# Optimization experiments

Hardware: AMD Instinct MI355X
Metric: run time of the kernel (lower is better)

The kernel has to match this reference:

```python
import jax, jax.numpy as jnp
import numpy as np

H = 16           # num_heads
D = 1024         # hidden_size
HD = D // H      # head_dim = 64
LN_EPS = 1e-5


def setup_inputs() -> dict:
    key = jax.random.key(0)
    ks = jax.random.split(key, 11)
    s = 1.0 / np.sqrt(D)
    x = jax.random.normal(ks[0], (2, 2048, D), dtype=jnp.float32)
    Wq = jax.random.uniform(ks[1], (D, D), jnp.float32, -s, s)
    bq = jax.random.uniform(ks[2], (D,), jnp.float32, -s, s)
    Wk = jax.random.uniform(ks[3], (D, D), jnp.float32, -s, s)
    bk = jax.random.uniform(ks[4], (D,), jnp.float32, -s, s)
    Wv = jax.random.uniform(ks[5], (D, D), jnp.float32, -s, s)
    bv = jax.random.uniform(ks[6], (D,), jnp.float32, -s, s)
    Wo = jax.random.uniform(ks[7], (D, D), jnp.float32, -s, s)
    bo = jax.random.uniform(ks[8], (D,), jnp.float32, -s, s)
    gamma = jnp.ones((D,), jnp.float32)
    beta = jnp.zeros((D,), jnp.float32)
    return {"x": x, "Wq": Wq, "bq": bq, "Wk": Wk, "bk": bk,
            "Wv": Wv, "bv": bv, "Wo": Wo, "bo": bo,
            "gamma": gamma, "beta": beta}


def reference(x, Wq, bq, Wk, bk, Wv, bv, Wo, bo, gamma, beta):
    B, S, _ = x.shape
    # projections -> [B, H, S, HD]
    def split_heads(t):
        return t.reshape(B, S, H, HD).transpose(0, 2, 1, 3)
    Q = split_heads(x @ Wq + bq)
    K = split_heads(x @ Wk + bk)
    V = split_heads(x @ Wv + bv)
    # scores [B, H, S, S], softmax over keys (dropout = identity in eval)
    scores = jnp.einsum('bhqd,bhkd->bhqk', Q, K) / np.sqrt(HD).astype(np.float32)
    attn = jax.nn.softmax(scores, axis=-1)
    ctx = jnp.einsum('bhqk,bhkd->bhqd', attn, V)          # [B, H, S, HD]
    ctx = ctx.transpose(0, 2, 1, 3).reshape(B, S, H * HD)  # [B, S, D]
    out = ctx @ Wo + bo
    # residual + LayerNorm
    y = out + x
    mu = jnp.mean(y, axis=-1, keepdims=True)
    var = jnp.mean(jnp.square(y - mu), axis=-1, keepdims=True)
    return (y - mu) * jax.lax.rsqrt(var + LN_EPS) * gamma + beta
```

## Files before the change

### kernel.cpp

```cpp
#include <hip/hip_runtime.h>
#include <cstdint>
#include <cstddef>


typedef short  b16x8  __attribute__((ext_vector_type(8)));
typedef float  f32x4  __attribute__((ext_vector_type(4)));
typedef float  f32x16 __attribute__((ext_vector_type(16)));

#define AS1 __attribute__((address_space(1)))
#define AS3 __attribute__((address_space(3)))

__device__ __forceinline__ unsigned short f2bf(float f) {
    unsigned int u = __builtin_bit_cast(unsigned int, f);
    u += 0x7FFFu + ((u >> 16) & 1u);
    return (unsigned short)(u >> 16);
}

__device__ __forceinline__ unsigned int cvt_pk_bf16(float lo, float hi) {
    unsigned int r;
    asm("v_cvt_pk_bf16_f32 %0, %1, %2" : "=v"(r) : "v"(lo), "v"(hi));
    return r;
}

__device__ __forceinline__ float exp2_fast(float x) {
    float r;
    asm("v_exp_f32 %0, %1" : "=v"(r) : "v"(x));
    return r;
}

__device__ __forceinline__ void permswap(unsigned &a, unsigned &b) {
    asm volatile("v_permlane32_swap_b32 %0, %1" : "+v"(a), "+v"(b));
}

__global__ __launch_bounds__(256) void k_cvt_x(const float* __restrict__ x,
                                               unsigned short* __restrict__ xb) {
    int i = blockIdx.x * 256 + threadIdx.x;
    size_t base = (size_t)i * 8;
    float4 v0 = *(const float4*)(x + base);
    float4 v1 = *(const float4*)(x + base + 4);
    int row = (int)(base >> 10), col = (int)(base & 1023);
    int rt = row >> 7, rr = row & 127, kt = col >> 6, cc = col & 63;
    int e = (rr * 64 + cc) ^ ((rr & 7) << 3);
    unsigned short o[8];
    o[0] = f2bf(v0.x); o[1] = f2bf(v0.y); o[2] = f2bf(v0.z); o[3] = f2bf(v0.w);
    o[4] = f2bf(v1.x); o[5] = f2bf(v1.y); o[6] = f2bf(v1.z); o[7] = f2bf(v1.w);
    *(uint4*)(xb + (size_t)(rt * 16 + kt) * 8192 + e) = *(uint4*)o;
}

__global__ __launch_bounds__(1024) void k_cvt_w(
    const float* __restrict__ W0, const float* __restrict__ W1,
    const float* __restrict__ W2, const float* __restrict__ W3,
    unsigned short* __restrict__ T0, unsigned short* __restrict__ T1,
    unsigned short* __restrict__ T2, unsigned short* __restrict__ T3) {
    const float* W = blockIdx.z == 0 ? W0 : blockIdx.z == 1 ? W1 : blockIdx.z == 2 ? W2 : W3;
    unsigned short* T = blockIdx.z == 0 ? T0 : blockIdx.z == 1 ? T1 : blockIdx.z == 2 ? T2 : T3;
    __shared__ float tile[32][33];
    int k0 = blockIdx.x * 32, n0 = blockIdx.y * 32;
    int tx = threadIdx.x, ty = threadIdx.y;
    tile[ty][tx] = W[(size_t)(k0 + ty) * 1024 + n0 + tx];
    __syncthreads();
    int n = n0 + ty, k = k0 + tx;
    unsigned short v = f2bf(tile[tx][ty]);
    if (blockIdx.z == 3) {
        T[(size_t)n * 1024 + k] = v;
    } else {
        int r = n & 127, c = k & 63;
        int e = (r * 64 + c) ^ ((r & 7) << 3);
        T[(size_t)((n >> 7) * 16 + (k >> 6)) * 8192 + e] = v;
    }
}

__global__ __launch_bounds__(512) void k_gemm_qkv(
    const unsigned short* __restrict__ A, const unsigned short* __restrict__ Bt,
    const float* __restrict__ bq, const float* __restrict__ bk, const float* __restrict__ bv,
    unsigned short* __restrict__ Qb, unsigned short* __restrict__ Kt,
    unsigned short* __restrict__ Vt) {
    __shared__ unsigned short As[3][8192];
    __shared__ unsigned short Bs[3][8192];
    const int tid = threadIdx.x, lane = tid & 63, wid = tid >> 6;
    const int m0 = blockIdx.y * 128, n0 = blockIdx.x * 128;
    const int wr = wid >> 2, wc = wid & 3;
    const int g = lane >> 4, r = lane & 15;
    f32x4 acc[4][2] = {};

    const unsigned short* Abase = A  + (size_t)blockIdx.y * 16 * 8192;
    const unsigned short* Bbase = Bt + (size_t)blockIdx.x * 16 * 8192;

#define GSTAGE(kt, buf) do {                                                              \
        const unsigned short* _a = Abase + (size_t)(kt) * 8192 + tid * 8;                 \
        const unsigned short* _b = Bbase + (size_t)(kt) * 8192 + tid * 8;                 \
        __builtin_amdgcn_global_load_lds((const AS1 void*)(_a),        (AS3 void*)((char*)As[buf] + tid * 16),        16, 0, 0); \
        __builtin_amdgcn_global_load_lds((const AS1 void*)(_a + 4096), (AS3 void*)((char*)As[buf] + 8192 + tid * 16), 16, 0, 0); \
        __builtin_amdgcn_global_load_lds((const AS1 void*)(_b),        (AS3 void*)((char*)Bs[buf] + tid * 16),        16, 0, 0); \
        __builtin_amdgcn_global_load_lds((const AS1 void*)(_b + 4096), (AS3 void*)((char*)Bs[buf] + 8192 + tid * 16), 16, 0, 0); \
    } while (0)

    GSTAGE(0, 0);
    GSTAGE(1, 1);
    asm volatile("s_waitcnt vmcnt(4)" ::: "memory");
    __builtin_amdgcn_s_barrier();
    __builtin_amdgcn_sched_barrier(0);

    for (int kt = 0; kt < 16; ++kt) {
        const unsigned short* Ac = As[kt % 3];
        const unsigned short* Bc = Bs[kt % 3];
        if (kt < 14) GSTAGE(kt + 2, (kt + 2) % 3);
#pragma unroll
        for (int kk = 0; kk < 2; ++kk) {
            b16x8 af[4], bfr[2];
#pragma unroll
            for (int mi = 0; mi < 4; ++mi) {
                int row = wr * 64 + mi * 16 + r;
                int e = (row * 64 + kk * 32 + g * 8) ^ ((row & 7) << 3);
                af[mi] = __builtin_bit_cast(b16x8, *(const uint4*)(Ac + e));
            }
#pragma unroll
            for (int ni = 0; ni < 2; ++ni) {
                int row = wc * 32 + ni * 16 + r;
                int e = (row * 64 + kk * 32 + g * 8) ^ ((row & 7) << 3);
                bfr[ni] = __builtin_bit_cast(b16x8, *(const uint4*)(Bc + e));
            }
#pragma unroll
            for (int mi = 0; mi < 4; ++mi)
#pragma unroll
                for (int ni = 0; ni < 2; ++ni)
                    acc[mi][ni] = __builtin_amdgcn_mfma_f32_16x16x32_bf16(af[mi], bfr[ni], acc[mi][ni], 0, 0, 0);
        }
        asm volatile("s_waitcnt lgkmcnt(0)" ::: "memory");
        if (kt < 15) {
            if (kt < 14) asm volatile("s_waitcnt vmcnt(4)" ::: "memory");
            else         asm volatile("s_waitcnt vmcnt(0)" ::: "memory");
            __builtin_amdgcn_s_barrier();
            __builtin_amdgcn_sched_barrier(0);
        }
    }
#undef GSTAGE

    for (int ni = 0; ni < 2; ++ni) {
        int col = n0 + wc * 32 + ni * 16 + r;
        int which = col >> 10, c = col & 1023;
        const float* bp = which == 0 ? bq : which == 1 ? bk : bv;
        float bvv = bp[c];
        int h = c >> 6, hd = c & 63;
        for (int mi = 0; mi < 4; ++mi)
            for (int j = 0; j < 4; ++j) {
                int row = m0 + wr * 64 + mi * 16 + g * 4 + j;
                float v = acc[mi][ni][j] + bvv;
                int b = row >> 11, s = row & 2047;
                size_t bh = (size_t)(b * 16 + h);
                if (which == 0) {
                    Qb[(bh * 2048 + s) * 64 + hd] = f2bf(v * 0.180336881f);
                } else if (which == 1) {
                    int tt = s >> 6, kr = s & 63;
                    Kt[(bh * 32 + tt) * 4096 + ((kr * 64 + hd) ^ ((kr & 7) << 3))] = f2bf(v);
                } else {
                    int tt = s >> 6, cc = s & 63;
                    Vt[(bh * 32 + tt) * 4096 + ((hd * 64 + cc) ^ ((hd & 7) << 3))] = f2bf(v);
                }
            }
    }
}

__global__ __launch_bounds__(512) void k_gemm_proj(
    const unsigned short* __restrict__ A, const unsigned short* __restrict__ Bt,
    const float* __restrict__ bias, float* __restrict__ out) {
    __shared__ unsigned short As[2][128 * 32];
    __shared__ unsigned short Bs[2][64 * 32];
    const int tid = threadIdx.x, lane = tid & 63, wid = tid >> 6;
    const int m0 = blockIdx.y * 128, n0 = blockIdx.x * 64;
    const int wr = wid >> 1, wc = wid & 1;
    f32x4 acc[2][2] = {};

    const int srow = tid >> 2, scol = (tid & 3) * 8;
    const unsigned short* Ag = A  + (size_t)(m0 + srow) * 1024 + scol;
    const unsigned short* Bg = Bt + (size_t)(n0 + srow) * 1024 + scol;

#define PSTAGE(kt, buf) do {                                                              \
        __builtin_amdgcn_global_load_lds((const AS1 void*)(Ag + (kt) * 32),               \
                                         (AS3 void*)((char*)As[buf] + tid * 16), 16, 0, 0); \
        if (tid < 256)                                                                    \
            __builtin_amdgcn_global_load_lds((const AS1 void*)(Bg + (kt) * 32),           \
                                             (AS3 void*)((char*)Bs[buf] + tid * 16), 16, 0, 0); \
    } while (0)

    PSTAGE(0, 0);
    __syncthreads();

    const int g = lane >> 4, r = lane & 15;
    for (int kt = 0; kt < 32; ++kt) {
        const int cur = kt & 1;
        if (kt < 31) PSTAGE(kt + 1, cur ^ 1);
        b16x8 af[2], bfr[2];
#pragma unroll
        for (int mi = 0; mi < 2; ++mi)
            af[mi] = __builtin_bit_cast(b16x8, *(const uint4*)(As[cur] + (wr * 32 + mi * 16 + r) * 32 + g * 8));
#pragma unroll
        for (int ni = 0; ni < 2; ++ni)
            bfr[ni] = __builtin_bit_cast(b16x8, *(const uint4*)(Bs[cur] + (wc * 32 + ni * 16 + r) * 32 + g * 8));
#pragma unroll
        for (int mi = 0; mi < 2; ++mi)
#pragma unroll
            for (int ni = 0; ni < 2; ++ni)
                acc[mi][ni] = __builtin_amdgcn_mfma_f32_16x16x32_bf16(af[mi], bfr[ni], acc[mi][ni], 0, 0, 0);
        __syncthreads();
    }
#undef PSTAGE

    for (int mi = 0; mi < 2; ++mi)
        for (int ni = 0; ni < 2; ++ni) {
            int col = n0 + wc * 32 + ni * 16 + r;
            float bv = bias[col];
            for (int j = 0; j < 4; ++j) {
                int row = m0 + wr * 32 + mi * 16 + g * 4 + j;
                out[(size_t)row * 1024 + col] = acc[mi][ni][j] + bv;
            }
        }
}

#define TSWZ(row, byteoff) ((((row) * 128) + (byteoff)) ^ (((row) & 7) << 4))

__global__ __launch_bounds__(512, 4) void k_attn(const unsigned short* __restrict__ Qb,
                                                 const unsigned short* __restrict__ Kt,
                                                 const unsigned short* __restrict__ Vt,
                                                 unsigned short* __restrict__ ctx) {
    __shared__ unsigned short Ks[2][2][4096];
    __shared__ unsigned short Vs[2][2][4096];
    __shared__ float lsh[4][64];
    const int tid = threadIdx.x, lane = tid & 63, w = tid >> 6;
    const int q32 = lane & 31, hi = lane >> 5;
    const int wq = w & 3, grp = w >> 2;
    const int lt = wq * 64 + lane;

    int bid = blockIdx.x;
    int xcd = bid & 7, idx = bid >> 3;
    int bh = xcd * 4 + (idx & 3);
    int q0 = (idx >> 2) * 128;
    const int b = bh >> 4, h = bh & 15;

    const unsigned short* qrow = Qb + ((size_t)bh * 2048 + q0 + wq * 32 + q32) * 64 + hi * 8;
    b16x8 qf[4];
#pragma unroll
    for (int ds = 0; ds < 4; ++ds)
        qf[ds] = __builtin_bit_cast(b16x8, *(const uint4*)(qrow + ds * 16));

    const unsigned short* Kg = Kt + (size_t)bh * 32 * 4096;
    const unsigned short* Vg = Vt + (size_t)bh * 32 * 4096;
    const int ktbase = grp * 16;

#define STAGE(i, buf) do {                                                                \
        const unsigned short* _ks = Kg + (size_t)(ktbase + (i)) * 4096 + lt * 8;          \
        const unsigned short* _vs = Vg + (size_t)(ktbase + (i)) * 4096 + lt * 8;          \
        __builtin_amdgcn_global_load_lds((const AS1 void*)_ks,          (AS3 void*)((char*)Ks[grp][buf] + lt * 16),        16, 0, 0); \
        __builtin_amdgcn_global_load_lds((const AS1 void*)(_ks + 2048), (AS3 void*)((char*)Ks[grp][buf] + 4096 + lt * 16), 16, 0, 0); \
        __builtin_amdgcn_global_load_lds((const AS1 void*)_vs,          (AS3 void*)((char*)Vs[grp][buf] + lt * 16),        16, 0, 0); \
        __builtin_amdgcn_global_load_lds((const AS1 void*)(_vs + 2048), (AS3 void*)((char*)Vs[grp][buf] + 4096 + lt * 16), 16, 0, 0); \
    } while (0)

    float lpart = 0.f;
    f32x16 oacc[2] = {};

    STAGE(0, 0);
    __syncthreads();

    for (int i = 0; i < 16; ++i) {
        const int cur = i & 1;
        if (i < 15) STAGE(i + 1, cur ^ 1);

        f32x16 sacc[2] = {};
#pragma unroll
        for (int ds = 0; ds < 4; ++ds) {
            b16x8 kf0 = __builtin_bit_cast(b16x8, *(const uint4*)((char*)Ks[grp][cur] + TSWZ(q32,      ds * 32 + hi * 16)));
            b16x8 kf1 = __builtin_bit_cast(b16x8, *(const uint4*)((char*)Ks[grp][cur] + TSWZ(32 + q32, ds * 32 + hi * 16)));
            sacc[0] = __builtin_amdgcn_mfma_f32_32x32x16_bf16(kf0, qf[ds], sacc[0], 0, 0, 0);
            sacc[1] = __builtin_amdgcn_mfma_f32_32x32x16_bf16(kf1, qf[ds], sacc[1], 0, 0, 0);
        }

        float pb[2][16];
#pragma unroll
        for (int kb = 0; kb < 2; ++kb)
#pragma unroll
            for (int reg = 0; reg < 16; ++reg)
                pb[kb][reg] = exp2_fast(sacc[kb][reg]);
        {
            float t0 = (pb[0][0]  + pb[0][1])  + (pb[0][2]  + pb[0][3]);
            float t1 = (pb[0][4]  + pb[0][5])  + (pb[0][6]  + pb[0][7]);
            float t2 = (pb[0][8]  + pb[0][9])  + (pb[0][10] + pb[0][11]);
            float t3 = (pb[0][12] + pb[0][13]) + (pb[0][14] + pb[0][15]);
            float t4 = (pb[1][0]  + pb[1][1])  + (pb[1][2]  + pb[1][3]);
            float t5 = (pb[1][4]  + pb[1][5])  + (pb[1][6]  + pb[1][7]);
            float t6 = (pb[1][8]  + pb[1][9])  + (pb[1][10] + pb[1][11]);
            float t7 = (pb[1][12] + pb[1][13]) + (pb[1][14] + pb[1][15]);
            lpart += ((t0 + t1) + (t2 + t3)) + ((t4 + t5) + (t6 + t7));
        }
        unsigned wv[2][4][2];
#pragma unroll
        for (int kb = 0; kb < 2; ++kb)
#pragma unroll
            for (int rg = 0; rg < 4; ++rg) {
                wv[kb][rg][0] = cvt_pk_bf16(pb[kb][rg * 4 + 0], pb[kb][rg * 4 + 1]);
                wv[kb][rg][1] = cvt_pk_bf16(pb[kb][rg * 4 + 2], pb[kb][rg * 4 + 3]);
            }
        b16x8 pa[4];
#pragma unroll
        for (int ks = 0; ks < 4; ++ks) {
            int kb = ks >> 1, rg0 = (ks & 1) * 2;
            unsigned u0 = wv[kb][rg0][0], u2 = wv[kb][rg0 + 1][0];
            permswap(u0, u2);
            unsigned u1 = wv[kb][rg0][1], u3 = wv[kb][rg0 + 1][1];
            permswap(u1, u3);
            uint4 uu; uu.x = u0; uu.y = u1; uu.z = u2; uu.w = u3;
            pa[ks] = __builtin_bit_cast(b16x8, uu);
        }
#pragma unroll
        for (int ks = 0; ks < 4; ++ks) {
            b16x8 vf0 = __builtin_bit_cast(b16x8, *(const uint4*)((char*)Vs[grp][cur] + TSWZ(q32,      ks * 32 + hi * 16)));
            b16x8 vf1 = __builtin_bit_cast(b16x8, *(const uint4*)((char*)Vs[grp][cur] + TSWZ(32 + q32, ks * 32 + hi * 16)));
            oacc[0] = __builtin_amdgcn_mfma_f32_32x32x16_bf16(pa[ks], vf0, oacc[0], 0, 0, 0);
            oacc[1] = __builtin_amdgcn_mfma_f32_32x32x16_bf16(pa[ks], vf1, oacc[1], 0, 0, 0);
        }
        __syncthreads();
    }

    {
        unsigned a = __builtin_bit_cast(unsigned, lpart), bb = a;
        permswap(a, bb);
        lpart = __builtin_bit_cast(float, a) + __builtin_bit_cast(float, bb);
    }

    float* s0 = (float*)Ks[1];
    float* s1 = (float*)Vs[1];
    if (grp == 1) {
        int base = (wq * 64 + lane) * 16;
#pragma unroll
        for (int reg = 0; reg < 16; ++reg) {
            s0[base + reg] = oacc[0][reg];
            s1[base + reg] = oacc[1][reg];
        }
        lsh[wq][lane] = lpart;
    }
    __syncthreads();
    if (grp == 0) {
        float l = lpart + lsh[wq][lane];
        float inv = 1.f / l;
        int base = (wq * 64 + lane) * 16;
#pragma unroll
        for (int reg = 0; reg < 16; ++reg) {
            int qr = (reg & 3) + 8 * (reg >> 2) + 4 * hi;
            float iv = __shfl(inv, qr, 64);
            float o0 = (oacc[0][reg] + s0[base + reg]) * iv;
            float o1 = (oacc[1][reg] + s1[base + reg]) * iv;
            unsigned short* dst = ctx + ((size_t)(b * 2048 + q0 + wq * 32 + qr)) * 1024 + h * 64 + q32;
            dst[0]  = f2bf(o0);
            dst[32] = f2bf(o1);
        }
    }
#undef STAGE
}

__global__ __launch_bounds__(256) void k_ln(const float* __restrict__ proj,
                                            const float* __restrict__ x,
                                            const float* __restrict__ gamma,
                                            const float* __restrict__ beta,
                                            float* __restrict__ out) {
    int t = threadIdx.x, lane = t & 63, w = t >> 6;
    int row = blockIdx.x * 4 + w;
    const float4* pr = (const float4*)(proj + (size_t)row * 1024);
    const float4* xr = (const float4*)(x    + (size_t)row * 1024);
    float4 y[4];
    float s = 0.f, ss = 0.f;
#pragma unroll
    for (int i = 0; i < 4; ++i) {
        float4 a = pr[lane + i * 64], bx = xr[lane + i * 64];
        float4 yy;
        yy.x = a.x + bx.x; yy.y = a.y + bx.y; yy.z = a.z + bx.z; yy.w = a.w + bx.w;
        y[i] = yy;
        s  += yy.x + yy.y + yy.z + yy.w;
        ss += yy.x * yy.x + yy.y * yy.y + yy.z * yy.z + yy.w * yy.w;
    }
#pragma unroll
    for (int o = 32; o > 0; o >>= 1) {
        s  += __shfl_xor(s,  o, 64);
        ss += __shfl_xor(ss, o, 64);
    }
    float mu  = s * (1.f / 1024.f);
    float var = ss * (1.f / 1024.f) - mu * mu;
    float inv = rsqrtf(var + 1e-5f);
    float4* outr = (float4*)(out + (size_t)row * 1024);
    const float4* gr = (const float4*)gamma;
    const float4* br = (const float4*)beta;
#pragma unroll
    for (int i = 0; i < 4; ++i) {
        float4 g4 = gr[lane + i * 64], b4 = br[lane + i * 64];
        float4 o4;
        o4.x = (y[i].x - mu) * inv * g4.x + b4.x;
        o4.y = (y[i].y - mu) * inv * g4.y + b4.y;
        o4.z = (y[i].z - mu) * inv * g4.z + b4.z;
        o4.w = (y[i].w - mu) * inv * g4.w + b4.w;
        outr[lane + i * 64] = o4;
    }
}

extern "C" void kernel_launch(void* const* d_in, const int* in_sizes, int n_in,
                              void* d_out, int out_size, void* d_ws, size_t ws_size,
                              hipStream_t stream) {
    const float* x  = (const float*)d_in[0];
    const float* Wq = (const float*)d_in[1];
    const float* bq = (const float*)d_in[2];
    const float* Wk = (const float*)d_in[3];
    const float* bk = (const float*)d_in[4];
    const float* Wv = (const float*)d_in[5];
    const float* bv = (const float*)d_in[6];
    const float* Wo = (const float*)d_in[7];
    const float* bo = (const float*)d_in[8];
    const float* gamma = (const float*)d_in[9];
    const float* beta  = (const float*)d_in[10];

    char* ws = (char*)d_ws;
    const size_t MB = 1u << 20;
    unsigned short* xbf   = (unsigned short*)(ws);
    unsigned short* Wqkvt = (unsigned short*)(ws + 8 * MB);
    unsigned short* Wot   = (unsigned short*)(ws + 14 * MB);
    unsigned short* Qb    = (unsigned short*)(ws + 16 * MB);
    unsigned short* Kt    = (unsigned short*)(ws + 24 * MB);
    unsigned short* Vt    = (unsigned short*)(ws + 32 * MB);
    float* proj = (float*)(ws + 16 * MB);
    unsigned short* ctx = xbf;

    k_cvt_x<<<2048, 256, 0, stream>>>(x, xbf);
    k_cvt_w<<<dim3(32, 32, 4), dim3(32, 32), 0, stream>>>(
        Wq, Wk, Wv, Wo, Wqkvt, Wqkvt + 1024 * 1024, Wqkvt + 2 * 1024 * 1024, Wot);
    k_gemm_qkv<<<dim3(24, 32), 512, 0, stream>>>(xbf, Wqkvt, bq, bk, bv, Qb, Kt, Vt);
    k_attn<<<512, 512, 0, stream>>>(Qb, Kt, Vt, ctx);
    k_gemm_proj<<<dim3(16, 32), 512, 0, stream>>>(ctx, Wot, bo, proj);
    k_ln<<<1024, 256, 0, stream>>>(proj, x, gamma, beta, (float*)d_out);
}
```

Before: 128.8 us.

## Restructure output projection GEMM with swizzled tiled layout and fused residual

The output projection GEMM now uses 128x128 tiles with a three-stage global-to-LDS pipeline over pre-tiled, XOR-swizzled operands, matching the QKV GEMM design. To feed it, the attention kernel writes ctx in the tiled swizzled layout and Wo is converted into the same tiled format. The residual add of x moves into the GEMM epilogue, so the LayerNorm kernel reads one tensor instead of two. The trade-off is fewer blocks (256 instead of 512), which lowers occupancy, and ctx stores from attention that are more scattered.

Result: faster. 124.1 us (-3.6%).

```diff
diff --git a/kernel.cpp b/kernel.cpp
--- a/kernel.cpp
+++ b/kernel.cpp
@@ -61,13 +61,9 @@
     __syncthreads();
     int n = n0 + ty, k = k0 + tx;
     unsigned short v = f2bf(tile[tx][ty]);
-    if (blockIdx.z == 3) {
-        T[(size_t)n * 1024 + k] = v;
-    } else {
-        int r = n & 127, c = k & 63;
-        int e = (r * 64 + c) ^ ((r & 7) << 3);
-        T[(size_t)((n >> 7) * 16 + (k >> 6)) * 8192 + e] = v;
-    }
+    int r = n & 127, c = k & 63;
+    int e = (r * 64 + c) ^ ((r & 7) << 3);
+    T[(size_t)((n >> 7) * 16 + (k >> 6)) * 8192 + e] = v;
 }
 
 __global__ __launch_bounds__(512) void k_gemm_qkv(
@@ -163,58 +159,79 @@
 
 __global__ __launch_bounds__(512) void k_gemm_proj(
     const unsigned short* __restrict__ A, const unsigned short* __restrict__ Bt,
-    const float* __restrict__ bias, float* __restrict__ out) {
-    __shared__ unsigned short As[2][128 * 32];
-    __shared__ unsigned short Bs[2][64 * 32];
+    const float* __restrict__ bias, const float* __restrict__ x,
+    float* __restrict__ out) {
+    __shared__ unsigned short As[3][8192];
+    __shared__ unsigned short Bs[3][8192];
     const int tid = threadIdx.x, lane = tid & 63, wid = tid >> 6;
-    const int m0 = blockIdx.y * 128, n0 = blockIdx.x * 64;
-    const int wr = wid >> 1, wc = wid & 1;
-    f32x4 acc[2][2] = {};
-
-    const int srow = tid >> 2, scol = (tid & 3) * 8;
-    const unsigned short* Ag = A  + (size_t)(m0 + srow) * 1024 + scol;
-    const unsigned short* Bg = Bt + (size_t)(n0 + srow) * 1024 + scol;
+    const int m0 = blockIdx.y * 128, n0 = blockIdx.x * 128;
+    const int wr = wid >> 2, wc = wid & 3;
+    const int g = lane >> 4, r = lane & 15;
+    f32x4 acc[4][2] = {};
+
+    const unsigned short* Abase = A  + (size_t)blockIdx.y * 16 * 8192;
+    const unsigned short* Bbase = Bt + (size_t)blockIdx.x * 16 * 8192;
 
 #define PSTAGE(kt, buf) do {                                                              \
-        __builtin_amdgcn_global_load_lds((const AS1 void*)(Ag + (kt) * 32),               \
-                                         (AS3 void*)((char*)As[buf] + tid * 16), 16, 0, 0); \
-        if (tid < 256)                                                                    \
-            __builtin_amdgcn_global_load_lds((const AS1 void*)(Bg + (kt) * 32),           \
-                                             (AS3 void*)((char*)Bs[buf] + tid * 16), 16, 0, 0); \
+        const unsigned short* _a = Abase + (size_t)(kt) * 8192 + tid * 8;                 \
+        const unsigned short* _b = Bbase + (size_t)(kt) * 8192 + tid * 8;                 \
+        __builtin_amdgcn_global_load_lds((const AS1 void*)(_a),        (AS3 void*)((char*)As[buf] + tid * 16),        16, 0, 0); \
+        __builtin_amdgcn_global_load_lds((const AS1 void*)(_a + 4096), (AS3 void*)((char*)As[buf] + 8192 + tid * 16), 16, 0, 0); \
+        __builtin_amdgcn_global_load_lds((const AS1 void*)(_b),        (AS3 void*)((char*)Bs[buf] + tid * 16),        16, 0, 0); \
+        __builtin_amdgcn_global_load_lds((const AS1 void*)(_b + 4096), (AS3 void*)((char*)Bs[buf] + 8192 + tid * 16), 16, 0, 0); \
     } while (0)
 
     PSTAGE(0, 0);
-    __syncthreads();
-
-    const int g = lane >> 4, r = lane & 15;
-    for (int kt = 0; kt < 32; ++kt) {
-        const int cur = kt & 1;
-        if (kt < 31) PSTAGE(kt + 1, cur ^ 1);
-        b16x8 af[2], bfr[2];
-#pragma unroll
-        for (int mi = 0; mi < 2; ++mi)
-            af[mi] = __builtin_bit_cast(b16x8, *(const uint4*)(As[cur] + (wr * 32 + mi * 16 + r) * 32 + g * 8));
-#pragma unroll
-        for (int ni = 0; ni < 2; ++ni)
-            bfr[ni] = __builtin_bit_cast(b16x8, *(const uint4*)(Bs[cur] + (wc * 32 + ni * 16 + r) * 32 + g * 8));
-#pragma unroll
-        for (int mi = 0; mi < 2; ++mi)
-#pragma unroll
-            for (int ni = 0; ni < 2; ++ni)
-                acc[mi][ni] = __builtin_amdgcn_mfma_f32_16x16x32_bf16(af[mi], bfr[ni], acc[mi][ni], 0, 0, 0);
-        __syncthreads();
+    PSTAGE(1, 1);
+    asm volatile("s_waitcnt vmcnt(4)" ::: "memory");
+    __builtin_amdgcn_s_barrier();
+    __builtin_amdgcn_sched_barrier(0);
+
+    for (int kt = 0; kt < 16; ++kt) {
+        const unsigned short* Ac = As[kt % 3];
+        const unsigned short* Bc = Bs[kt % 3];
+        if (kt < 14) PSTAGE(kt + 2, (kt + 2) % 3);
+#pragma unroll
+        for (int kk = 0; kk < 2; ++kk) {
+            b16x8 af[4], bfr[2];
+#pragma unroll
+            for (int mi = 0; mi < 4; ++mi) {
+                int row = wr * 64 + mi * 16 + r;
+                int e = (row * 64 + kk * 32 + g * 8) ^ ((row & 7) << 3);
+                af[mi] = __builtin_bit_cast(b16x8, *(const uint4*)(Ac + e));
+            }
+#pragma unroll
+            for (int ni = 0; ni < 2; ++ni) {
+                int row = wc * 32 + ni * 16 + r;
+                int e = (row * 64 + kk * 32 + g * 8) ^ ((row & 7) << 3);
+                bfr[ni] = __builtin_bit_cast(b16x8, *(const uint4*)(Bc + e));
+            }
+#pragma unroll
+            for (int mi = 0; mi < 4; ++mi)
+#pragma unroll
+                for (int ni = 0; ni < 2; ++ni)
+                    acc[mi][ni] = __builtin_amdgcn_mfma_f32_16x16x32_bf16(af[mi], bfr[ni], acc[mi][ni], 0, 0, 0);
+        }
+        asm volatile("s_waitcnt lgkmcnt(0)" ::: "memory");
+        if (kt < 15) {
+            if (kt < 14) asm volatile("s_waitcnt vmcnt(4)" ::: "memory");
+            else         asm volatile("s_waitcnt vmcnt(0)" ::: "memory");
+            __builtin_amdgcn_s_barrier();
+            __builtin_amdgcn_sched_barrier(0);
+        }
     }
 #undef PSTAGE
 
-    for (int mi = 0; mi < 2; ++mi)
-        for (int ni = 0; ni < 2; ++ni) {
-            int col = n0 + wc * 32 + ni * 16 + r;
-            float bv = bias[col];
+    for (int ni = 0; ni < 2; ++ni) {
+        int col = n0 + wc * 32 + ni * 16 + r;
+        float bv = bias[col];
+        for (int mi = 0; mi < 4; ++mi)
             for (int j = 0; j < 4; ++j) {
-                int row = m0 + wr * 32 + mi * 16 + g * 4 + j;
-                out[(size_t)row * 1024 + col] = acc[mi][ni][j] + bv;
-            }
-        }
+                int row = m0 + wr * 64 + mi * 16 + g * 4 + j;
+                size_t off = (size_t)row * 1024 + col;
+                out[off] = acc[mi][ni][j] + bv + x[off];
+            }
+    }
 }
 
 #define TSWZ(row, byteoff) ((((row) * 128) + (byteoff)) ^ (((row) & 7) << 4))
@@ -349,30 +366,28 @@
             float iv = __shfl(inv, qr, 64);
             float o0 = (oacc[0][reg] + s0[base + reg]) * iv;
             float o1 = (oacc[1][reg] + s1[base + reg]) * iv;
-            unsigned short* dst = ctx + ((size_t)(b * 2048 + q0 + wq * 32 + qr)) * 1024 + h * 64 + q32;
-            dst[0]  = f2bf(o0);
-            dst[32] = f2bf(o1);
+            int row = b * 2048 + q0 + wq * 32 + qr;
+            int rt = row >> 7, rr = row & 127;
+            size_t tbase = (size_t)(rt * 16 + h) * 8192;
+            ctx[tbase + ((rr * 64 + q32)      ^ ((rr & 7) << 3))] = f2bf(o0);
+            ctx[tbase + ((rr * 64 + q32 + 32) ^ ((rr & 7) << 3))] = f2bf(o1);
         }
     }
 #undef STAGE
 }
 
-__global__ __launch_bounds__(256) void k_ln(const float* __restrict__ proj,
-                                            const float* __restrict__ x,
+__global__ __launch_bounds__(256) void k_ln(const float* __restrict__ yin,
                                             const float* __restrict__ gamma,
                                             const float* __restrict__ beta,
                                             float* __restrict__ out) {
     int t = threadIdx.x, lane = t & 63, w = t >> 6;
     int row = blockIdx.x * 4 + w;
-    const float4* pr = (const float4*)(proj + (size_t)row * 1024);
-    const float4* xr = (const float4*)(x    + (size_t)row * 1024);
+    const float4* yr = (const float4*)(yin + (size_t)row * 1024);
     float4 y[4];
     float s = 0.f, ss = 0.f;
 #pragma unroll
     for (int i = 0; i < 4; ++i) {
-        float4 a = pr[lane + i * 64], bx = xr[lane + i * 64];
-        float4 yy;
-        yy.x = a.x + bx.x; yy.y = a.y + bx.y; yy.z = a.z + bx.z; yy.w = a.w + bx.w;
+        float4 yy = yr[lane + i * 64];
         y[i] = yy;
         s  += yy.x + yy.y + yy.z + yy.w;
         ss += yy.x * yy.x + yy.y * yy.y + yy.z * yy.z + yy.w * yy.w;
@@ -431,6 +446,6 @@
         Wq, Wk, Wv, Wo, Wqkvt, Wqkvt + 1024 * 1024, Wqkvt + 2 * 1024 * 1024, Wot);
     k_gemm_qkv<<<dim3(24, 32), 512, 0, stream>>>(xbf, Wqkvt, bq, bk, bv, Qb, Kt, Vt);
     k_attn<<<512, 512, 0, stream>>>(Qb, Kt, Vt, ctx);
-    k_gemm_proj<<<dim3(16, 32), 512, 0, stream>>>(ctx, Wot, bo, proj);
-    k_ln<<<1024, 256, 0, stream>>>(proj, x, gamma, beta, (float*)d_out);
-}
+    k_gemm_proj<<<dim3(8, 32), 512, 0, stream>>>(ctx, Wot, bo, x, proj);
+    k_ln<<<1024, 256, 0, stream>>>(proj, gamma, beta, (float*)d_out);
+}
```
